# Optimization experiments

Hardware: AMD Instinct MI355X
Metric: run time of the kernel (lower is better)

Reference implementation:

```python
import jax, jax.numpy as jnp
import numpy as np

B, NH, T, N, D = 4, 8, 2048, 512, 128
THETA = 2.0 ** 16
GAMMA = 0.995


def setup_inputs() -> dict:
    key = jax.random.key(0)
    kq, kv, ks = jax.random.split(key, 3)
    Q = jax.random.normal(kq, (B, NH, T, N), jnp.float32)
    V = jax.random.normal(kv, (B, NH, T, D), jnp.float32)
    S_prev = 0.01 * jax.random.normal(ks, (B, NH, N, D), jnp.float32)
    # get_freqs(N, theta=2**16): per-channel inverse frequencies
    freqs = jnp.asarray(1.0 / THETA ** (np.arange(N, dtype=np.float32) / N), jnp.float32)
    gamma = jnp.float32(GAMMA)
    return {"Q": Q, "V": V, "S_prev": S_prev, "freqs": freqs, "gamma": gamma}


def _rope(phases, v):
    """Rotary embedding with per-channel phases. phases broadcasts against v's
    last two dims (T, N); rotate-half formulation."""
    cos, sin = jnp.cos(phases), jnp.sin(phases)
    half = v.shape[-1] // 2
    v_rot = jnp.concatenate([-v[..., half:], v[..., :half]], axis=-1)
    return v * cos + v_rot * sin


def reference(Q, V, S_prev, freqs, gamma):
    # Q: (B,nh,T,N)  V: (B,nh,T,D)  S_prev: (B,nh,N,D)
    t_len = Q.shape[2]
    phases = jnp.arange(t_len, dtype=freqs.dtype)[:, None] * freqs[None, :]  # (T,N)
    QR = _rope(phases[None, None], Q)  # K == Q per the module's assert

    q_seq = jnp.moveaxis(QR, 2, 0)  # (T,B,nh,N)
    v_seq = jnp.moveaxis(V, 2, 0)   # (T,B,nh,D)

    def step(S, qv):
        q_t, v_t = qv
        out_t = jnp.einsum('bhn,bhnd->bhd', q_t, S)          # read before write
        S_new = (S + jnp.einsum('bhn,bhd->bhnd', q_t, v_t)) * gamma  # write + decay
        return S_new, out_t

    S_final, outs = jax.lax.scan(step, S_prev, (q_seq, v_seq))
    output = jnp.moveaxis(outs, 0, 2)  # (B,nh,T,D)
    return output, S_final
```

## Files before the change

kernel.cpp:

```cpp
#include <hip/hip_runtime.h>
#include <hip/hip_bf16.h>

typedef __attribute__((ext_vector_type(8))) short short8;
typedef __attribute__((ext_vector_type(4))) float f32x4;

#define MFMA16(a,b,c) __builtin_amdgcn_mfma_f32_16x16x32_bf16((a),(b),(c),0,0,0)

constexpr int BHn = 32;
constexpr int Tn  = 2048;
constexpr int Nn  = 512;
constexpr int Dn  = 128;
constexpr int CHn = 64;
constexpr int NCH = Tn / CHn;

static __device__ __forceinline__ unsigned short f2b(float x){
  __hip_bfloat16 h = __float2bfloat16(x);
  return *reinterpret_cast<unsigned short*>(&h);
}

__global__ __launch_bounds__(256) void rope_k(const float* __restrict__ Q,
                                              const float* __restrict__ freqs,
                                              unsigned short* __restrict__ QR){
  int gid = blockIdx.x * 256 + threadIdx.x;
  int np  = gid & 255;
  int t   = gid >> 8;
  float tf = (float)t;
  float f1 = freqs[np], f2 = freqs[np + 256];
  float s1, c1, s2, c2;
  sincosf(tf * f1, &s1, &c1);
  sincosf(tf * f2, &s2, &c2);
  size_t off = (size_t)t * Nn + np;
  for (int bh = 0; bh < BHn; ++bh){
    size_t base = (size_t)bh * Tn * Nn + off;
    float q1 = Q[base], q2 = Q[base + 256];
    QR[base]       = f2b(q1 * c1 - q2 * s1);
    QR[base + 256] = f2b(q2 * c2 + q1 * s2);
  }
}

__device__ __forceinline__ short8 ldfrag(const unsigned short* buf, int rowbase, int k0, int ld, int lane){
  int row = rowbase + (lane & 15);
  int col = (k0 + ((lane >> 4) << 3)) ^ ((row & 7) << 3);
  return *reinterpret_cast<const short8*>(buf + row * ld + col);
}

__device__ __forceinline__ void stage_Rs(unsigned short* Rs, uint4 a, uint4 b, int dt, int n0){
  *reinterpret_cast<uint4*>(&Rs[ dt      * 512 + (n0 ^ (( dt      & 7) << 3))]) = a;
  *reinterpret_cast<uint4*>(&Rs[(dt + 1) * 512 + (n0 ^ (((dt + 1) & 7) << 3))]) = b;
}

__global__ __launch_bounds__(512, 1) void lattn_main(
    const unsigned short* __restrict__ QR,
    const float* __restrict__ V,
    const float* __restrict__ S_prev,
    const float* __restrict__ gammap,
    float* __restrict__ Out,
    float* __restrict__ Sfin)
{
  __shared__ __align__(16) unsigned short Rs [64 * 512];
  __shared__ __align__(16) unsigned short SbTs[16 * 512];
  __shared__ __align__(16) unsigned short VTs[2][16 * 64];
  __shared__ __align__(16) unsigned short Ps [64 * 64];
  __shared__ float gpow[65], gpinv[65];

  const int tid  = threadIdx.x;
  const int w    = tid >> 6;
  const int lane = tid & 63;
  const int bh   = blockIdx.x & 31;
  const int dch  = blockIdx.x >> 5;
  const int d0   = dch * 16;
  const float g  = gammap[0];

  const unsigned short* QRbh = QR + (size_t)bh * Tn * Nn;
  const float* Vbh = V + (size_t)bh * Tn * Dn;

  if (tid < 65){
    gpow[tid]  = powf(g,  (float)tid);
    gpinv[tid] = powf(g, -(float)tid);
  }
  #pragma unroll
  for (int i = tid; i < 64 * 64; i += 512) Ps[i] = 0;

  f32x4 st[8];
  if (w >= 4){
    int r0 = (w - 4) * 8;
    #pragma unroll
    for (int j = 0; j < 8; ++j){
      int n = (r0 + j) * 16 + (lane & 15);
      const float* sp = S_prev + (size_t)bh * Nn * Dn + (size_t)n * Dn + d0 + ((lane >> 4) << 2);
      st[j] = *reinterpret_cast<const f32x4*>(sp);
    }
  }
  __syncthreads();
  const float g64 = gpow[64];

  {
    #pragma unroll
    for (int i = 0; i < 4; ++i){
      int p  = tid + i * 512;
      int dt = (p >> 6) << 1;
      int n0 = (p & 63) << 3;
      const unsigned short* src = QRbh + (size_t)dt * Nn + n0;
      uint4 a = *reinterpret_cast<const uint4*>(src);
      uint4 b = *reinterpret_cast<const uint4*>(src + Nn);
      stage_Rs(Rs, a, b, dt, n0);
    }
    {
      int dtv = tid >> 3, dp = (tid & 7) << 1;
      const float* vp = Vbh + (size_t)dtv * Dn + d0 + dp;
      float sc = gpinv[dtv];
      VTs[0][ dp      * 64 + (dtv ^ (( dp      & 7) << 3))] = f2b(vp[0] * sc);
      VTs[0][(dp + 1) * 64 + (dtv ^ (((dp + 1) & 7) << 3))] = f2b(vp[1] * sc);
    }
    if (w >= 4){
      int r0 = (w - 4) * 8;
      #pragma unroll
      for (int j = 0; j < 8; ++j){
        int n  = (r0 + j) * 16 + (lane & 15);
        int dl = (lane >> 4) << 2;
        #pragma unroll
        for (int r = 0; r < 4; ++r){
          int d = dl + r;
          SbTs[d * 512 + (n ^ ((d & 7) << 3))] = f2b(st[j][r]);
        }
      }
    }
  }
  __syncthreads();

  for (int c = 0; c < NCH; ++c){
    const int t0 = c * CHn;
    const int vb = c & 1;
    const bool pf = (c + 1 < NCH);

    uint4 ra[4], rb[4];
    float va0 = 0.f, va1 = 0.f;
    const int n0_  = (tid & 63) << 3;
    const int dtv_ = tid >> 3;
    if (pf){
      const unsigned short* QRc = QRbh + (size_t)(t0 + CHn) * Nn;
      #pragma unroll
      for (int i = 0; i < 4; ++i){
        int dt = (((tid >> 6) + 8 * i) << 1);
        const unsigned short* src = QRc + (size_t)dt * Nn + n0_;
        ra[i] = *reinterpret_cast<const uint4*>(src);
        rb[i] = *reinterpret_cast<const uint4*>(src + Nn);
      }
      const float* vp = Vbh + (size_t)(t0 + CHn + dtv_) * Dn + d0 + ((tid & 7) << 1);
      va0 = vp[0]; va1 = vp[1];
    }

    f32x4 oacc = {0.f, 0.f, 0.f, 0.f};
    if (w < 4){
      f32x4 p0 = {0.f,0.f,0.f,0.f}, p1 = p0, p2 = p0;
      for (int kb = 0; kb < 16; ++kb){
        int k0 = kb * 32;
        short8 fs = ldfrag(SbTs, 0, k0, 512, lane);
        if (w == 0){
          short8 f0 = ldfrag(Rs,  0, k0, 512, lane);
          short8 f1 = ldfrag(Rs, 16, k0, 512, lane);
          p0   = MFMA16(f0, f0, p0);
          p1   = MFMA16(f1, f0, p1);
          p2   = MFMA16(f1, f1, p2);
          oacc = MFMA16(fs, f0, oacc);
        } else if (w == 1){
          short8 f0 = ldfrag(Rs,  0, k0, 512, lane);
          short8 f1 = ldfrag(Rs, 16, k0, 512, lane);
          short8 f2 = ldfrag(Rs, 32, k0, 512, lane);
          p0   = MFMA16(f2, f0, p0);
          p1   = MFMA16(f2, f1, p1);
          p2   = MFMA16(f2, f2, p2);
          oacc = MFMA16(fs, f2, oacc);
        } else if (w == 2){
          short8 f0 = ldfrag(Rs,  0, k0, 512, lane);
          short8 f1 = ldfrag(Rs, 16, k0, 512, lane);
          short8 f3 = ldfrag(Rs, 48, k0, 512, lane);
          p0   = MFMA16(f3, f0, p0);
          p1   = MFMA16(f3, f1, p1);
          oacc = MFMA16(fs, f3, oacc);
        } else {
          short8 f1 = ldfrag(Rs, 16, k0, 512, lane);
          short8 f2 = ldfrag(Rs, 32, k0, 512, lane);
          short8 f3 = ldfrag(Rs, 48, k0, 512, lane);
          p0   = MFMA16(f3, f2, p0);
          p1   = MFMA16(f3, f3, p1);
          oacc = MFMA16(fs, f1, oacc);
        }
      }
      int tI[3], tJ[3], nt;
      if      (w == 0){ tI[0]=0; tJ[0]=0; tI[1]=1; tJ[1]=0; tI[2]=1; tJ[2]=1; nt = 3; }
      else if (w == 1){ tI[0]=2; tJ[0]=0; tI[1]=2; tJ[1]=1; tI[2]=2; tJ[2]=2; nt = 3; }
      else if (w == 2){ tI[0]=3; tJ[0]=0; tI[1]=3; tJ[1]=1; tI[2]=0; tJ[2]=0; nt = 2; }
      else            { tI[0]=3; tJ[0]=2; tI[1]=3; tJ[1]=3; tI[2]=0; tJ[2]=0; nt = 2; }
      f32x4 pacc[3] = {p0, p1, p2};
      for (int q = 0; q < nt; ++q){
        int j  = tJ[q] * 16 + (lane & 15);
        int i0 = tI[q] * 16 + ((lane >> 4) << 2);
        #pragma unroll
        for (int r = 0; r < 4; ++r){
          int i = i0 + r;
          float v = (j < i) ? pacc[q][r] * gpow[i] : 0.f;
          Ps[i * 64 + (j ^ ((i & 7) << 3))] = f2b(v);
        }
      }
    } else {
      int r0 = (w - 4) * 8;
      #pragma unroll
      for (int ks = 0; ks < 2; ++ks){
        short8 av = ldfrag(VTs[vb], 0, ks * 32, 64, lane);
        #pragma unroll
        for (int j = 0; j < 8; ++j){
          int n = (r0 + j) * 16 + (lane & 15);
          short8 bn;
          #pragma unroll
          for (int e = 0; e < 8; ++e){
            int dt = ks * 32 + ((lane >> 4) << 3) + e;
            bn[e] = (short)Rs[dt * 512 + (n ^ (e << 3))];
          }
          st[j] = MFMA16(av, bn, st[j]);
        }
      }
      #pragma unroll
      for (int j = 0; j < 8; ++j)
        #pragma unroll
        for (int r = 0; r < 4; ++r) st[j][r] *= g64;
    }
    __syncthreads();

    if (w >= 4){
      int r0 = (w - 4) * 8;
      #pragma unroll
      for (int j = 0; j < 8; ++j){
        int n  = (r0 + j) * 16 + (lane & 15);
        int dl = (lane >> 4) << 2;
        #pragma unroll
        for (int r = 0; r < 4; ++r){
          int d = dl + r;
          SbTs[d * 512 + (n ^ ((d & 7) << 3))] = f2b(st[j][r]);
        }
      }
    } else {
      const int itl = (w == 0) ? 0 : (w == 1) ? 2 : (w == 2) ? 3 : 1;
      float gi = gpow[itl * 16 + (lane & 15)];
      #pragma unroll
      for (int r = 0; r < 4; ++r) oacc[r] *= gi;
      #pragma unroll
      for (int ks = 0; ks < 2; ++ks){
        short8 av = ldfrag(VTs[vb], 0, ks * 32, 64, lane);
        short8 bp = ldfrag(Ps, itl * 16, ks * 32, 64, lane);
        oacc = MFMA16(av, bp, oacc);
      }
      int ti = t0 + itl * 16 + (lane & 15);
      float* op = Out + (size_t)bh * Tn * Dn + (size_t)ti * Dn + d0 + ((lane >> 4) << 2);
      *reinterpret_cast<f32x4*>(op) = oacc;
    }
    if (pf){
      #pragma unroll
      for (int i = 0; i < 4; ++i){
        int dt = (((tid >> 6) + 8 * i) << 1);
        stage_Rs(Rs, ra[i], rb[i], dt, n0_);
      }
      int dp = (tid & 7) << 1;
      float sc = gpinv[dtv_];
      VTs[vb ^ 1][ dp      * 64 + (dtv_ ^ (( dp      & 7) << 3))] = f2b(va0 * sc);
      VTs[vb ^ 1][(dp + 1) * 64 + (dtv_ ^ (((dp + 1) & 7) << 3))] = f2b(va1 * sc);
    }
    __syncthreads();
  }

  if (w >= 4){
    int r0 = (w - 4) * 8;
    #pragma unroll
    for (int j = 0; j < 8; ++j){
      int n = (r0 + j) * 16 + (lane & 15);
      float* sp = Sfin + (size_t)bh * Nn * Dn + (size_t)n * Dn + d0 + ((lane >> 4) << 2);
      *reinterpret_cast<f32x4*>(sp) = st[j];
    }
  }
}

extern "C" void kernel_launch(void* const* d_in, const int* in_sizes, int n_in,
                              void* d_out, int out_size, void* d_ws, size_t ws_size,
                              hipStream_t stream){
  const float* Q      = (const float*)d_in[0];
  const float* V      = (const float*)d_in[1];
  const float* S_prev = (const float*)d_in[2];
  const float* freqs  = (const float*)d_in[3];
  const float* gamma  = (const float*)d_in[4];
  float* Out  = (float*)d_out;
  float* Sfin = Out + (size_t)BHn * Tn * Dn;
  unsigned short* QR = (unsigned short*)d_ws;

  rope_k<<<2048, 256, 0, stream>>>(Q, freqs, QR);
  lattn_main<<<256, 512, 0, stream>>>(QR, V, S_prev, gamma, Out, Sfin);
}
```

Measured before the change: 223.1 us.

## Read rotated Q fragments directly from global memory instead of LDS staging

Drops the 64KB LDS buffer for the rotated Q chunk and its register prefetch. MFMA fragments are now loaded straight from global memory (L2/L1), and the S-update warps gather transposed Q columns with strided 2-byte global loads. The k-loop is also fully unrolled. This saves LDS capacity and staging stores, but adds global-latency exposure and uncoalesced scalar gathers in the state-update path.

```diff
diff --git a/kernel.cpp b/kernel.cpp
--- a/kernel.cpp
+++ b/kernel.cpp
@@ -44,9 +44,9 @@
   return *reinterpret_cast<const short8*>(buf + row * ld + col);
 }
 
-__device__ __forceinline__ void stage_Rs(unsigned short* Rs, uint4 a, uint4 b, int dt, int n0){
-  *reinterpret_cast<uint4*>(&Rs[ dt      * 512 + (n0 ^ (( dt      & 7) << 3))]) = a;
-  *reinterpret_cast<uint4*>(&Rs[(dt + 1) * 512 + (n0 ^ (((dt + 1) & 7) << 3))]) = b;
+__device__ __forceinline__ short8 gfrag(const unsigned short* Qc, int rowbase, int k0, int lane){
+  return *reinterpret_cast<const short8*>(
+      Qc + (size_t)(rowbase + (lane & 15)) * Nn + k0 + ((lane >> 4) << 3));
 }
 
 __global__ __launch_bounds__(512, 1) void lattn_main(
@@ -57,7 +57,6 @@
     float* __restrict__ Out,
     float* __restrict__ Sfin)
 {
-  __shared__ __align__(16) unsigned short Rs [64 * 512];
   __shared__ __align__(16) unsigned short SbTs[16 * 512];
   __shared__ __align__(16) unsigned short VTs[2][16 * 64];
   __shared__ __align__(16) unsigned short Ps [64 * 64];
@@ -95,23 +94,11 @@
   const float g64 = gpow[64];
 
   {
-    #pragma unroll
-    for (int i = 0; i < 4; ++i){
-      int p  = tid + i * 512;
-      int dt = (p >> 6) << 1;
-      int n0 = (p & 63) << 3;
-      const unsigned short* src = QRbh + (size_t)dt * Nn + n0;
-      uint4 a = *reinterpret_cast<const uint4*>(src);
-      uint4 b = *reinterpret_cast<const uint4*>(src + Nn);
-      stage_Rs(Rs, a, b, dt, n0);
-    }
-    {
-      int dtv = tid >> 3, dp = (tid & 7) << 1;
-      const float* vp = Vbh + (size_t)dtv * Dn + d0 + dp;
-      float sc = gpinv[dtv];
-      VTs[0][ dp      * 64 + (dtv ^ (( dp      & 7) << 3))] = f2b(vp[0] * sc);
-      VTs[0][(dp + 1) * 64 + (dtv ^ (((dp + 1) & 7) << 3))] = f2b(vp[1] * sc);
-    }
+    int dtv = tid >> 3, dp = (tid & 7) << 1;
+    const float* vp = Vbh + (size_t)dtv * Dn + d0 + dp;
+    float sc = gpinv[dtv];
+    VTs[0][ dp      * 64 + (dtv ^ (( dp      & 7) << 3))] = f2b(vp[0] * sc);
+    VTs[0][(dp + 1) * 64 + (dtv ^ (((dp + 1) & 7) << 3))] = f2b(vp[1] * sc);
     if (w >= 4){
       int r0 = (w - 4) * 8;
       #pragma unroll
@@ -132,20 +119,11 @@
     const int t0 = c * CHn;
     const int vb = c & 1;
     const bool pf = (c + 1 < NCH);
-
-    uint4 ra[4], rb[4];
+    const unsigned short* Qc = QRbh + (size_t)t0 * Nn;
+
     float va0 = 0.f, va1 = 0.f;
-    const int n0_  = (tid & 63) << 3;
     const int dtv_ = tid >> 3;
     if (pf){
-      const unsigned short* QRc = QRbh + (size_t)(t0 + CHn) * Nn;
-      #pragma unroll
-      for (int i = 0; i < 4; ++i){
-        int dt = (((tid >> 6) + 8 * i) << 1);
-        const unsigned short* src = QRc + (size_t)dt * Nn + n0_;
-        ra[i] = *reinterpret_cast<const uint4*>(src);
-        rb[i] = *reinterpret_cast<const uint4*>(src + Nn);
-      }
       const float* vp = Vbh + (size_t)(t0 + CHn + dtv_) * Dn + d0 + ((tid & 7) << 1);
       va0 = vp[0]; va1 = vp[1];
     }
@@ -153,35 +131,36 @@
     f32x4 oacc = {0.f, 0.f, 0.f, 0.f};
     if (w < 4){
       f32x4 p0 = {0.f,0.f,0.f,0.f}, p1 = p0, p2 = p0;
+      #pragma unroll
       for (int kb = 0; kb < 16; ++kb){
         int k0 = kb * 32;
         short8 fs = ldfrag(SbTs, 0, k0, 512, lane);
         if (w == 0){
-          short8 f0 = ldfrag(Rs,  0, k0, 512, lane);
-          short8 f1 = ldfrag(Rs, 16, k0, 512, lane);
+          short8 f0 = gfrag(Qc,  0, k0, lane);
+          short8 f1 = gfrag(Qc, 16, k0, lane);
           p0   = MFMA16(f0, f0, p0);
           p1   = MFMA16(f1, f0, p1);
           p2   = MFMA16(f1, f1, p2);
           oacc = MFMA16(fs, f0, oacc);
         } else if (w == 1){
-          short8 f0 = ldfrag(Rs,  0, k0, 512, lane);
-          short8 f1 = ldfrag(Rs, 16, k0, 512, lane);
-          short8 f2 = ldfrag(Rs, 32, k0, 512, lane);
+          short8 f0 = gfrag(Qc,  0, k0, lane);
+          short8 f1 = gfrag(Qc, 16, k0, lane);
+          short8 f2 = gfrag(Qc, 32, k0, lane);
           p0   = MFMA16(f2, f0, p0);
           p1   = MFMA16(f2, f1, p1);
           p2   = MFMA16(f2, f2, p2);
           oacc = MFMA16(fs, f2, oacc);
         } else if (w == 2){
-          short8 f0 = ldfrag(Rs,  0, k0, 512, lane);
-          short8 f1 = ldfrag(Rs, 16, k0, 512, lane);
-          short8 f3 = ldfrag(Rs, 48, k0, 512, lane);
+          short8 f0 = gfrag(Qc,  0, k0, lane);
+          short8 f1 = gfrag(Qc, 16, k0, lane);
+          short8 f3 = gfrag(Qc, 48, k0, lane);
           p0   = MFMA16(f3, f0, p0);
           p1   = MFMA16(f3, f1, p1);
           oacc = MFMA16(fs, f3, oacc);
         } else {
-          short8 f1 = ldfrag(Rs, 16, k0, 512, lane);
-          short8 f2 = ldfrag(Rs, 32, k0, 512, lane);
-          short8 f3 = ldfrag(Rs, 48, k0, 512, lane);
+          short8 f1 = gfrag(Qc, 16, k0, lane);
+          short8 f2 = gfrag(Qc, 32, k0, lane);
+          short8 f3 = gfrag(Qc, 48, k0, lane);
           p0   = MFMA16(f3, f2, p0);
           p1   = MFMA16(f3, f3, p1);
           oacc = MFMA16(fs, f1, oacc);
@@ -211,12 +190,10 @@
         #pragma unroll
         for (int j = 0; j < 8; ++j){
           int n = (r0 + j) * 16 + (lane & 15);
+          const unsigned short* col = Qc + (size_t)(ks * 32 + ((lane >> 4) << 3)) * Nn + n;
           short8 bn;
           #pragma unroll
-          for (int e = 0; e < 8; ++e){
-            int dt = ks * 32 + ((lane >> 4) << 3) + e;
-            bn[e] = (short)Rs[dt * 512 + (n ^ (e << 3))];
-          }
+          for (int e = 0; e < 8; ++e) bn[e] = (short)col[(size_t)e * Nn];
           st[j] = MFMA16(av, bn, st[j]);
         }
       }
@@ -255,11 +232,6 @@
       *reinterpret_cast<f32x4*>(op) = oacc;
     }
     if (pf){
-      #pragma unroll
-      for (int i = 0; i < 4; ++i){
-        int dt = (((tid >> 6) + 8 * i) << 1);
-        stage_Rs(Rs, ra[i], rb[i], dt, n0_);
-      }
       int dp = (tid & 7) << 1;
       float sc = gpinv[dtv_];
       VTs[vb ^ 1][ dp      * 64 + (dtv_ ^ (( dp      & 7) << 3))] = f2b(va0 * sc);
```

Result: slower. 301.9 us (+35.3%).
